# Kernel tuning notes

Measured on AMD Instinct MI355X. Metric: run time of the kernel, lower is better.

The kernel has to match this reference:

```python
import jax, jax.numpy as jnp
import numpy as np
from jax import lax

B, C, L = 32, 64, 16384
C_OUT = 64


def conv1d(x, w, b):
    # x: [B,C,L], w: [Cout,Cin,K], b: [Cout]
    y = lax.conv_general_dilated(x, w, window_strides=(1,), padding='VALID',
                                 dimension_numbers=('NCH', 'OIH', 'NCH'))
    return y + b[None, :, None]


def setup_inputs() -> dict:
    key = jax.random.key(0)
    k1, k2, k3, k4, k5 = jax.random.split(key, 5)
    x = jax.random.normal(k1, (B, C, L), dtype=jnp.float32)
    # kernel_size = 1 (see shape_source); PyTorch Conv1d default init scale ~ 1/sqrt(Cin*K)
    s = 1.0 / np.sqrt(C * 1)
    offset_w = jax.random.uniform(k2, (C * 1, C, 1), jnp.float32, -s, s)
    offset_b = jax.random.uniform(k3, (C * 1,), jnp.float32, -s, s)
    regular_w = jax.random.uniform(k4, (C_OUT, C, 1), jnp.float32, -s, s)
    regular_b = jax.random.uniform(k5, (C_OUT,), jnp.float32, -s, s)
    return {'x': x, 'offset_w': offset_w, 'offset_b': offset_b,
            'regular_w': regular_w, 'regular_b': regular_b}


def reference(x, offset_w, offset_b, regular_w, regular_b):
    Bx, Cx, Lx = x.shape
    offsets = conv1d(x, offset_w, offset_b)                 # [B,C,L]
    base = jnp.arange(Lx, dtype=x.dtype)[None, None, :]      # [1,1,L]
    indices = jnp.clip(base + offsets, 0.0, Lx - 1)          # [B,C,L] float positions
    idx_floor = jnp.floor(indices)
    idx_ceil = jnp.ceil(indices)
    x_floor = jnp.take_along_axis(x, idx_floor.astype(jnp.int32), axis=2)
    x_ceil = jnp.take_along_axis(x, idx_ceil.astype(jnp.int32), axis=2)
    frac = indices - idx_floor
    x_deform = (1.0 - frac) * x_floor + frac * x_ceil        # [B,C,L]
    return conv1d(x_deform, regular_w, regular_b)            # [B,Cout,L]
```

## Files before the change

kernel.cpp:

```cpp
#include <hip/hip_runtime.h>


#define BDIM 256
#define BB   32
#define CC   64
#define LL   16384
#define TL   64
#define HH   4
#define ROWS (TL + 2*HH)
#define RSW  36
#define RSH  72
#define NT   4
#define XTB  10368

typedef __fp16 half_t;
typedef __attribute__((ext_vector_type(2))) __fp16 h2;
typedef __attribute__((ext_vector_type(8))) __fp16 h8;
typedef __attribute__((ext_vector_type(4))) float f4;

union H2U { h2 h; unsigned u; };
union H8U { unsigned u[4]; h8 v; };

static __device__ __forceinline__ unsigned pk(float a, float b) {
    H2U r; r.h = __builtin_amdgcn_cvt_pkrtz(a, b); return r.u;
}

static __device__ __forceinline__ void load_a_split(const float* __restrict__ wp,
                                                    int row, int ks, int q,
                                                    h8* ahi, h8* alo) {
    const float* base = wp + row * 64 + ks * 32 + q * 8;
    float4 w0 = *(const float4*)base;
    float4 w1 = *(const float4*)(base + 4);
    float v[8] = {w0.x, w0.y, w0.z, w0.w, w1.x, w1.y, w1.z, w1.w};
    H8U h, l;
    #pragma unroll
    for (int p = 0; p < 4; ++p) {
        H2U hh; hh.h = __builtin_amdgcn_cvt_pkrtz(v[2*p], v[2*p+1]);
        h.u[p] = hh.u;
        l.u[p] = pk(v[2*p] - (float)hh.h[0], v[2*p+1] - (float)hh.h[1]);
    }
    *ahi = h.v; *alo = l.v;
}

static __device__ __forceinline__ h8 load_a_f16(const float* __restrict__ wp,
                                                int row, int ks, int q) {
    const float* base = wp + row * 64 + ks * 32 + q * 8;
    float4 w0 = *(const float4*)base;
    float4 w1 = *(const float4*)(base + 4);
    float v[8] = {w0.x, w0.y, w0.z, w0.w, w1.x, w1.y, w1.z, w1.w};
    H8U r;
    #pragma unroll
    for (int p = 0; p < 4; ++p) r.u[p] = pk(v[2*p], v[2*p+1]);
    return r.v;
}

static __device__ __forceinline__ void stage_write4(unsigned* dst, int cb, int rowb,
                                                    const float4& v0, const float4& v1,
                                                    const float4& v2, const float4& v3) {
    float a0[4] = {v0.x, v0.y, v0.z, v0.w};
    float a1[4] = {v1.x, v1.y, v1.z, v1.w};
    float a2[4] = {v2.x, v2.y, v2.z, v2.w};
    float a3[4] = {v3.x, v3.y, v3.z, v3.w};
    int wbase = rowb * RSW + (((cb >> 1) ^ ((rowb >> 2) & 7)) << 2) + 2 * (cb & 1);
    #pragma unroll
    for (int rl = 0; rl < 4; ++rl) {
        uint2 hw;
        hw.x = pk(a0[rl], a1[rl]);
        hw.y = pk(a2[rl], a3[rl]);
        *(uint2*)&dst[wbase + rl * RSW] = hw;
    }
}

__global__ __launch_bounds__(BDIM)
void deform_conv1d_r6(const float* __restrict__ x,
                      const float* __restrict__ offw,
                      const float* __restrict__ offb,
                      const float* __restrict__ regw,
                      const float* __restrict__ regb,
                      float* __restrict__ out) {
    __shared__ __align__(16) unsigned char smem[2 * XTB + 9216];
    unsigned* XdW = (unsigned*)(smem + 2 * XTB);

    const int tid = threadIdx.x;
    const int bx  = blockIdx.x;
    const int b   = blockIdx.y;
    const size_t xb = (size_t)b * CC * LL;

    const int wv   = tid >> 6;
    const int lane = tid & 63;
    const int q    = lane >> 4;
    const int n    = lane & 15;
    const int scb  = tid >> 4;
    const int slb  = tid & 15;

    {
        const int lg0 = (NT * bx) * TL;
        unsigned* dst = (unsigned*)smem;
        half_t*  dsth = (half_t*)smem;
        if (bx == 0) {
            for (int i = tid; i < ROWS * CC; i += BDIM) {
                int r = i >> 6, c = i & 63;
                int g = min(max(lg0 - HH + r, 0), LL - 1);
                float v = x[xb + (size_t)c * LL + g];
                int blk = (c >> 3) ^ ((r >> 2) & 7);
                dsth[r * RSH + (blk << 3) + (c & 7)] = (half_t)v;
            }
        } else {
            const float* pp = x + xb + (size_t)(4 * scb) * LL + (lg0 + 4 + 4 * slb);
            float4 v0 = *(const float4*)pp;
            float4 v1 = *(const float4*)(pp + LL);
            float4 v2 = *(const float4*)(pp + 2 * LL);
            float4 v3 = *(const float4*)(pp + 3 * LL);
            stage_write4(dst, scb, 8 + 4 * slb, v0, v1, v2, v3);
            if (tid < 32) {
                int lb2 = tid & 1, cb2 = tid >> 1;
                const float* p2 = x + xb + (size_t)(4 * cb2) * LL + (lg0 - 4 + 4 * lb2);
                float4 u0 = *(const float4*)p2;
                float4 u1 = *(const float4*)(p2 + LL);
                float4 u2 = *(const float4*)(p2 + 2 * LL);
                float4 u3 = *(const float4*)(p2 + 3 * LL);
                stage_write4(dst, cb2, 4 * lb2, u0, u1, u2, u3);
            }
        }
    }

    h8 ahi[2], alo[2], a2f[2];
    load_a_split(offw, 16 * wv + n, 0, q, &ahi[0], &alo[0]);
    load_a_split(offw, 16 * wv + n, 1, q, &ahi[1], &alo[1]);
    a2f[0] = load_a_f16(regw, 16 * wv + n, 0, q);
    a2f[1] = load_a_f16(regw, 16 * wv + n, 1, q);
    float4 bo = *(const float4*)(offb + 16 * wv + 4 * q);
    float4 br = *(const float4*)(regb + 16 * wv + 4 * q);
    __syncthreads();

    #pragma unroll
    for (int tt = 0; tt < NT; ++tt) {
        const int lg0 = (NT * bx + tt) * TL;
        unsigned* Xc  = (unsigned*)(smem + (tt & 1) * XTB);
        unsigned* Xn  = (unsigned*)(smem + ((tt & 1) ^ 1) * XTB);
        half_t*   Xch = (half_t*)Xc;
        const bool has_next  = (tt < NT - 1);
        const bool next_fast = has_next && !(bx == 63 && tt == NT - 2);

        float4 s0, s1, s2, s3;
        if (next_fast) {
            const float* pp = x + xb + (size_t)(4 * scb) * LL + (lg0 + TL + 4 + 4 * slb);
            s0 = *(const float4*)pp;
            s1 = *(const float4*)(pp + LL);
            s2 = *(const float4*)(pp + 2 * LL);
            s3 = *(const float4*)(pp + 3 * LL);
        }

        f4 acc[4];
        #pragma unroll
        for (int nt = 0; nt < 4; ++nt) acc[nt] = (f4){bo.x, bo.y, bo.z, bo.w};
        #pragma unroll
        for (int nt = 0; nt < 4; ++nt) {
            const int r  = 16 * nt + n + HH;
            const int rb = r * RSW;
            const int sb = (r >> 2) & 7;
            #pragma unroll
            for (int ks = 0; ks < 2; ++ks) {
                int blk = (4 * ks + q) ^ sb;
                h8 bv = *(const h8*)&Xc[rb + (blk << 2)];
                acc[nt] = __builtin_amdgcn_mfma_f32_16x16x32_f16(ahi[ks], bv, acc[nt], 0, 0, 0);
                acc[nt] = __builtin_amdgcn_mfma_f32_16x16x32_f16(alo[ks], bv, acc[nt], 0, 0, 0);
            }
        }

        #pragma unroll
        for (int nt = 0; nt < 4; ++nt) {
            const int l = lg0 + 16 * nt + n;
            #pragma unroll
            for (int reg = 0; reg < 4; ++reg) {
                const int c = 16 * wv + 4 * q + reg;
                float o  = acc[nt][reg];
                float p  = (float)l + o;
                p = __builtin_amdgcn_fmed3f(p, 0.0f, (float)(LL - 1));
                float of = floorf(p);
                float fr = p - of;
                int idx  = (int)of;
                int u    = idx - lg0 + HH;
                float x0, x1;
                if ((unsigned)u <= (unsigned)(ROWS - 2)) {
                    int b0 = (c >> 3) ^ ((u >> 2) & 7);
                    int b1 = (c >> 3) ^ (((u + 1) >> 2) & 7);
                    x0 = (float)Xch[u * RSH + (b0 << 3) + (c & 7)];
                    x1 = (float)Xch[(u + 1) * RSH + (b1 << 3) + (c & 7)];
                } else {
                    const float* xr = x + xb + (size_t)c * LL;
                    x0 = xr[idx];
                    x1 = xr[idx + (fr > 0.0f ? 1 : 0)];
                }
                acc[nt][reg] = x0 + fr * (x1 - x0);
            }
        }

        #pragma unroll
        for (int nt = 0; nt < 4; ++nt) {
            const int row = 16 * nt + n;
            const int sb  = (row >> 2) & 7;
            const int bw  = (2 * wv + (q >> 1)) ^ sb;
            uint2 pw;
            pw.x = pk(acc[nt][0], acc[nt][1]);
            pw.y = pk(acc[nt][2], acc[nt][3]);
            *(uint2*)&XdW[row * RSW + (bw << 2) + 2 * (q & 1)] = pw;
        }

        if (has_next) {
            if (tid < 144) {
                int j  = tid / 18;
                int k2 = (tid - 18 * j) * 2;
                *(uint2*)&Xn[j * RSW + k2] = *(const uint2*)&Xc[(64 + j) * RSW + k2];
            }
            if (next_fast) {
                stage_write4(Xn, scb, 8 + 4 * slb, s0, s1, s2, s3);
            } else {
                half_t* Xnh = (half_t*)Xn;
                for (int i = tid; i < TL * CC; i += BDIM) {
                    int r = 8 + (i >> 6), c = i & 63;
                    int g = min(lg0 + TL - HH + r, LL - 1);
                    float v = x[xb + (size_t)c * LL + g];
                    int blk = (c >> 3) ^ ((r >> 2) & 7);
                    Xnh[r * RSH + (blk << 3) + (c & 7)] = (half_t)v;
                }
            }
        }
        __syncthreads();

        #pragma unroll
        for (int nt = 0; nt < 4; ++nt) acc[nt] = (f4){br.x, br.y, br.z, br.w};
        #pragma unroll
        for (int nt = 0; nt < 4; ++nt) {
            const int row = 16 * nt + n;
            const int sb  = (row >> 2) & 7;
            #pragma unroll
            for (int ks = 0; ks < 2; ++ks) {
                int blk = (4 * ks + q) ^ sb;
                h8 bv = *(const h8*)&XdW[row * RSW + (blk << 2)];
                acc[nt] = __builtin_amdgcn_mfma_f32_16x16x32_f16(a2f[ks], bv, acc[nt], 0, 0, 0);
            }
        }

        float* op = out + (size_t)b * CC * LL;
        #pragma unroll
        for (int nt = 0; nt < 4; ++nt) {
            #pragma unroll
            for (int reg = 0; reg < 4; ++reg) {
                op[(size_t)(16 * wv + 4 * q + reg) * LL + lg0 + 16 * nt + n] = acc[nt][reg];
            }
        }
        if (tt < NT - 1) __syncthreads();
    }
}

extern "C" void kernel_launch(void* const* d_in, const int* in_sizes, int n_in,
                              void* d_out, int out_size, void* d_ws, size_t ws_size,
                              hipStream_t stream) {
    const float* x    = (const float*)d_in[0];
    const float* offw = (const float*)d_in[1];
    const float* offb = (const float*)d_in[2];
    const float* regw = (const float*)d_in[3];
    const float* regb = (const float*)d_in[4];
    float* out = (float*)d_out;

    dim3 grid(LL / TL / NT, BB);
    deform_conv1d_r6<<<grid, dim3(BDIM), 0, stream>>>(x, offw, offb, regw, regb, out);
}
```

Measured before the change: 258.1 us.

## Software-pipeline second GEMM one tile behind and double-buffer deformed tile

The second (regular) convolution GEMM and its global store now run for the previous tile at the start of the next iteration, reading from a double-buffered deformed-x tile. This removes one __syncthreads per tile and lets the second matmul overlap the next tile's prefetch and offset GEMM. Tiles per block double, so the grid shrinks by half, and the loop is no longer forced to unroll. This adds more shared memory and gives fewer blocks, which may lower occupancy and parallelism.

```diff
diff --git a/kernel.cpp b/kernel.cpp
--- a/kernel.cpp
+++ b/kernel.cpp
@@ -10,8 +10,9 @@
 #define ROWS (TL + 2*HH)
 #define RSW  36
 #define RSH  72
-#define NT   4
-#define XTB  10368
+#define NT   8
+#define XTW  (ROWS * RSW)
+#define XDW  (TL * RSW)
 
 typedef __fp16 half_t;
 typedef __attribute__((ext_vector_type(2))) __fp16 h2;
@@ -71,20 +72,49 @@
     }
 }
 
+static __device__ __forceinline__ void mm2_store(const unsigned* __restrict__ Xd,
+                                                 const h8* a2f, const float4& br,
+                                                 float* __restrict__ op, int lg0,
+                                                 int wv, int q, int n) {
+    f4 acc[4];
+    #pragma unroll
+    for (int nt = 0; nt < 4; ++nt) acc[nt] = (f4){br.x, br.y, br.z, br.w};
+    #pragma unroll
+    for (int nt = 0; nt < 4; ++nt) {
+        const int row = 16 * nt + n;
+        const int sb  = (row >> 2) & 7;
+        #pragma unroll
+        for (int ks = 0; ks < 2; ++ks) {
+            int blk = (4 * ks + q) ^ sb;
+            h8 bv = *(const h8*)&Xd[row * RSW + (blk << 2)];
+            acc[nt] = __builtin_amdgcn_mfma_f32_16x16x32_f16(a2f[ks], bv, acc[nt], 0, 0, 0);
+        }
+    }
+    #pragma unroll
+    for (int nt = 0; nt < 4; ++nt) {
+        #pragma unroll
+        for (int reg = 0; reg < 4; ++reg) {
+            op[(size_t)(16 * wv + 4 * q + reg) * LL + lg0 + 16 * nt + n] = acc[nt][reg];
+        }
+    }
+}
+
 __global__ __launch_bounds__(BDIM)
-void deform_conv1d_r6(const float* __restrict__ x,
+void deform_conv1d_r7(const float* __restrict__ x,
                       const float* __restrict__ offw,
                       const float* __restrict__ offb,
                       const float* __restrict__ regw,
                       const float* __restrict__ regb,
                       float* __restrict__ out) {
-    __shared__ __align__(16) unsigned char smem[2 * XTB + 9216];
-    unsigned* XdW = (unsigned*)(smem + 2 * XTB);
+    __shared__ __align__(16) unsigned smem[2 * XTW + 2 * XDW];
+    unsigned* XT = smem;
+    unsigned* XD = smem + 2 * XTW;
 
     const int tid = threadIdx.x;
     const int bx  = blockIdx.x;
     const int b   = blockIdx.y;
     const size_t xb = (size_t)b * CC * LL;
+    float* op = out + (size_t)b * CC * LL;
 
     const int wv   = tid >> 6;
     const int lane = tid & 63;
@@ -95,8 +125,8 @@
 
     {
         const int lg0 = (NT * bx) * TL;
-        unsigned* dst = (unsigned*)smem;
-        half_t*  dsth = (half_t*)smem;
+        unsigned* dst = XT;
+        half_t*  dsth = (half_t*)XT;
         if (bx == 0) {
             for (int i = tid; i < ROWS * CC; i += BDIM) {
                 int r = i >> 6, c = i & 63;
@@ -133,14 +163,15 @@
     float4 br = *(const float4*)(regb + 16 * wv + 4 * q);
     __syncthreads();
 
-    #pragma unroll
     for (int tt = 0; tt < NT; ++tt) {
         const int lg0 = (NT * bx + tt) * TL;
-        unsigned* Xc  = (unsigned*)(smem + (tt & 1) * XTB);
-        unsigned* Xn  = (unsigned*)(smem + ((tt & 1) ^ 1) * XTB);
+        unsigned* Xc  = XT + (tt & 1) * XTW;
+        unsigned* Xn  = XT + ((tt & 1) ^ 1) * XTW;
         half_t*   Xch = (half_t*)Xc;
+        unsigned* XdC = XD + (tt & 1) * XDW;
+        unsigned* XdP = XD + ((tt & 1) ^ 1) * XDW;
         const bool has_next  = (tt < NT - 1);
-        const bool next_fast = has_next && !(bx == 63 && tt == NT - 2);
+        const bool next_fast = has_next && !(bx == 31 && tt == NT - 2);
 
         float4 s0, s1, s2, s3;
         if (next_fast) {
@@ -150,6 +181,8 @@
             s2 = *(const float4*)(pp + 2 * LL);
             s3 = *(const float4*)(pp + 3 * LL);
         }
+
+        if (tt > 0) mm2_store(XdP, a2f, br, op, lg0 - TL, wv, q, n);
 
         f4 acc[4];
         #pragma unroll
@@ -204,7 +237,7 @@
             uint2 pw;
             pw.x = pk(acc[nt][0], acc[nt][1]);
             pw.y = pk(acc[nt][2], acc[nt][3]);
-            *(uint2*)&XdW[row * RSW + (bw << 2) + 2 * (q & 1)] = pw;
+            *(uint2*)&XdC[row * RSW + (bw << 2) + 2 * (q & 1)] = pw;
         }
 
         if (has_next) {
@@ -227,31 +260,10 @@
             }
         }
         __syncthreads();
-
-        #pragma unroll
-        for (int nt = 0; nt < 4; ++nt) acc[nt] = (f4){br.x, br.y, br.z, br.w};
-        #pragma unroll
-        for (int nt = 0; nt < 4; ++nt) {
-            const int row = 16 * nt + n;
-            const int sb  = (row >> 2) & 7;
-            #pragma unroll
-            for (int ks = 0; ks < 2; ++ks) {
-                int blk = (4 * ks + q) ^ sb;
-                h8 bv = *(const h8*)&XdW[row * RSW + (blk << 2)];
-                acc[nt] = __builtin_amdgcn_mfma_f32_16x16x32_f16(a2f[ks], bv, acc[nt], 0, 0, 0);
-            }
-        }
-
-        float* op = out + (size_t)b * CC * LL;
-        #pragma unroll
-        for (int nt = 0; nt < 4; ++nt) {
-            #pragma unroll
-            for (int reg = 0; reg < 4; ++reg) {
-                op[(size_t)(16 * wv + 4 * q + reg) * LL + lg0 + 16 * nt + n] = acc[nt][reg];
-            }
-        }
-        if (tt < NT - 1) __syncthreads();
-    }
+    }
+
+    mm2_store(XD + ((NT - 1) & 1) * XDW, a2f, br, op,
+              (NT * bx + NT - 1) * TL, wv, q, n);
 }
 
 extern "C" void kernel_launch(void* const* d_in, const int* in_sizes, int n_in,
@@ -265,5 +277,5 @@
     float* out = (float*)d_out;
 
     dim3 grid(LL / TL / NT, BB);
-    deform_conv1d_r6<<<grid, dim3(BDIM), 0, stream>>>(x, offw, offb, regw, regb, out);
-}
+    deform_conv1d_r7<<<grid, dim3(BDIM), 0, stream>>>(x, offw, offb, regw, regb, out);
+}
```

After: 261.9 us. No clear change (+1.5%).
